# Kernel optimization log

Measured on AMD Instinct MI355X. Metric: run time of the kernel, lower is better.

Reference implementation:

```python
import jax, jax.numpy as jnp
import numpy as np

S = 64.0
M = 0.5
EPS = 1e-07
NORM_EPS = 1e-12  # matches torch F.normalize default eps
B, D, C = 512, 512, 64000


def _l2_normalize(a, axis=-1):
    n = jnp.sqrt(jnp.sum(a * a, axis=axis, keepdims=True))
    return a / jnp.maximum(n, NORM_EPS)


def setup_inputs() -> dict:
    key = jax.random.key(0)
    kx, ky, kw = jax.random.split(key, 3)
    x = jax.random.normal(kx, (B, D), dtype=jnp.float32)
    y = jax.random.randint(ky, (B,), 0, C, dtype=jnp.int64)
    # kaiming_uniform-ish init: bound = sqrt(6 / fan_in)
    bound = np.sqrt(6.0 / D).astype(np.float32)
    W = jax.random.uniform(kw, (C, D), dtype=jnp.float32, minval=-bound, maxval=bound)
    return {"x": x, "y": y, "W": W}


def reference(x, y, W):
    # cosine similarities: [B, C]
    theta = _l2_normalize(x) @ _l2_normalize(W).T
    # target logit per row
    tgt = jnp.take_along_axis(theta, y[:, None], axis=1)[:, 0]  # [B]
    numerator = S * jnp.cos(jnp.arccos(jnp.clip(tgt, -1.0 + EPS, 1.0 - EPS)) + M)
    # sum of exp(s*theta) over non-target classes (mask out target column)
    is_tgt = jnp.arange(C, dtype=y.dtype)[None, :] == y[:, None]  # [B, C]
    excl_sum = jnp.sum(jnp.where(is_tgt, 0.0, jnp.exp(S * theta)), axis=1)  # [B]
    denominator = jnp.exp(numerator) + excl_sum
    return -jnp.mean(numerator - jnp.log(denominator))
```

## Files before the change

### kernel.cpp

```cpp
#include <hip/hip_runtime.h>


#define B_N 512
#define D_N 512
#define C_N 64000
#define S_SCALE 64.0f
#define MARGIN 0.5f
#define EPS_C 1e-7f

typedef unsigned short ushort_t;
typedef __attribute__((ext_vector_type(8))) short short8;
typedef __attribute__((ext_vector_type(4))) float floatx4;

__device__ __forceinline__ ushort_t f2bf(float f) {
    unsigned int u = __float_as_uint(f);
    u += 0x7fffu + ((u >> 16) & 1u);
    return (ushort_t)(u >> 16);
}

__global__ void xprep_kernel(const float* __restrict__ x,
                             ushort_t* __restrict__ xn,
                             float* __restrict__ rowsum) {
    int b = blockIdx.x;
    int t = threadIdx.x;
    if (b == 128) {
        rowsum[t] = 0.0f;
        rowsum[t + 256] = 0.0f;
        return;
    }
    int row  = b * 4 + (t >> 6);
    int lane = t & 63;
    const float4* p = (const float4*)(x + (size_t)row * D_N);
    float4 v0 = p[lane];
    float4 v1 = p[lane + 64];
    float ss = v0.x*v0.x + v0.y*v0.y + v0.z*v0.z + v0.w*v0.w
             + v1.x*v1.x + v1.y*v1.y + v1.z*v1.z + v1.w*v1.w;
#pragma unroll
    for (int off = 32; off > 0; off >>= 1) ss += __shfl_xor(ss, off);
    float sc = 1.0f / fmaxf(sqrtf(ss), 1e-12f);
    ushort_t* dst = xn + (size_t)row * D_N;
    uint2 o0, o1;
    o0.x = (unsigned)f2bf(v0.x*sc) | ((unsigned)f2bf(v0.y*sc) << 16);
    o0.y = (unsigned)f2bf(v0.z*sc) | ((unsigned)f2bf(v0.w*sc) << 16);
    o1.x = (unsigned)f2bf(v1.x*sc) | ((unsigned)f2bf(v1.y*sc) << 16);
    o1.y = (unsigned)f2bf(v1.z*sc) | ((unsigned)f2bf(v1.w*sc) << 16);
    *(uint2*)(dst + lane * 4)       = o0;
    *(uint2*)(dst + 256 + lane * 4) = o1;
}

__device__ __forceinline__ void g2lds16(const ushort_t* g, ushort_t* l) {
    __builtin_amdgcn_global_load_lds(
        (const __attribute__((address_space(1))) void*)g,
        (__attribute__((address_space(3))) void*)l, 16, 0, 0);
}

__global__ __launch_bounds__(512, 2)
void gemm_fused_kernel(const float* __restrict__ W,
                       const ushort_t* __restrict__ xn,
                       const int* __restrict__ y,
                       float* __restrict__ rowsum,
                       float* __restrict__ tgt) {
    __shared__ ushort_t sW[64 * 512];
    __shared__ ushort_t sA[2 * 512 * 32];

    int t    = threadIdx.x;
    int lane = t & 63;
    int w    = t >> 6;
    int lq   = lane >> 4;
    int lc   = lane & 15;
    int cn0  = blockIdx.x * 64;

#pragma unroll
    for (int rr = 0; rr < 8; ++rr) {
        int row = w * 8 + rr;
        const float4* p = (const float4*)(W + (size_t)(cn0 + row) * D_N);
        float4 a = p[lane * 2];
        float4 b = p[lane * 2 + 1];
        float ss = a.x*a.x + a.y*a.y + a.z*a.z + a.w*a.w
                 + b.x*b.x + b.y*b.y + b.z*b.z + b.w*b.w;
#pragma unroll
        for (int off = 32; off > 0; off >>= 1) ss += __shfl_xor(ss, off);
        float sc = 1.0f / fmaxf(sqrtf(ss), 1e-12f);
        uint4 o;
        o.x = (unsigned)f2bf(a.x*sc) | ((unsigned)f2bf(a.y*sc) << 16);
        o.y = (unsigned)f2bf(a.z*sc) | ((unsigned)f2bf(a.w*sc) << 16);
        o.z = (unsigned)f2bf(b.x*sc) | ((unsigned)f2bf(b.y*sc) << 16);
        o.w = (unsigned)f2bf(b.z*sc) | ((unsigned)f2bf(b.w*sc) << 16);
        int kc = lane;
        int rs = row ^ (kc & 7);
        *((uint4*)(sW + kc * 512 + rs * 8)) = o;
    }

    const ushort_t* gA = xn + (size_t)(t >> 2) * D_N + (t & 3) * 8;
#pragma unroll
    for (int c = 0; c < 4; ++c)
        g2lds16(gA + (size_t)c * 128 * D_N, sA + (t + c * 512) * 8);
    __syncthreads();

    floatx4 acc[4][4];
#pragma unroll
    for (int i = 0; i < 4; i++)
#pragma unroll
        for (int j = 0; j < 4; j++) acc[i][j] = (floatx4){0.f, 0.f, 0.f, 0.f};

    int fragA_base = (w * 64 + lc) * 32 + lq * 8;

    for (int k = 0; k < 16; ++k) {
        int cur = (k & 1) * 16384;
        if (k < 15) {
            int nxt = ((k + 1) & 1) * 16384;
            int kk  = (k + 1) * 32;
#pragma unroll
            for (int c = 0; c < 4; ++c)
                g2lds16(gA + (size_t)c * 128 * D_N + kk,
                        sA + nxt + (t + c * 512) * 8);
        }
        short8 af[4], bfr[4];
#pragma unroll
        for (int tm = 0; tm < 4; tm++)
            af[tm] = *(const short8*)(sA + cur + fragA_base + tm * 512);
#pragma unroll
        for (int tn = 0; tn < 4; tn++) {
            int kc = k * 4 + lq;
            int rs = (tn * 16 + lc) ^ (kc & 7);
            bfr[tn] = *(const short8*)(sW + kc * 512 + rs * 8);
        }
#pragma unroll
        for (int tm = 0; tm < 4; tm++)
#pragma unroll
            for (int tn = 0; tn < 4; tn++)
                acc[tm][tn] = __builtin_amdgcn_mfma_f32_16x16x32_bf16(
                    af[tm], bfr[tn], acc[tm][tn], 0, 0, 0);
        __syncthreads();
    }

    float* rowacc = (float*)sA;
#pragma unroll
    for (int tm = 0; tm < 4; tm++) {
#pragma unroll
        for (int r = 0; r < 4; r++) {
            int lrow = w * 64 + tm * 16 + lq * 4 + r;
            int yv   = y[lrow];
            float esum = 0.0f;
#pragma unroll
            for (int tn = 0; tn < 4; tn++) {
                int gcol = cn0 + tn * 16 + lc;
                float theta = acc[tm][tn][r];
                if (gcol == yv) {
                    tgt[lrow] = theta;
                } else {
                    esum += __expf(S_SCALE * theta);
                }
            }
#pragma unroll
            for (int off = 1; off < 16; off <<= 1) esum += __shfl_xor(esum, off);
            if (lc == 0) rowacc[lrow] = esum;
        }
    }
    __syncthreads();
    atomicAdd(&rowsum[t], rowacc[t]);
}

__global__ void finalize_kernel(const float* __restrict__ rowsum,
                                const float* __restrict__ tgt,
                                float* __restrict__ out) {
    __shared__ float red[256];
    int t = threadIdx.x;
    float s = 0.0f;
    for (int r = t; r < B_N; r += 256) {
        float tv = tgt[r];
        tv = fminf(fmaxf(tv, -1.0f + EPS_C), 1.0f - EPS_C);
        float num = S_SCALE * cosf(acosf(tv) + MARGIN);
        float den = expf(num) + rowsum[r];
        s += num - logf(den);
    }
    red[t] = s;
    __syncthreads();
    for (int o = 128; o > 0; o >>= 1) {
        if (t < o) red[t] += red[t + o];
        __syncthreads();
    }
    if (t == 0) out[0] = -red[0] / (float)B_N;
}

extern "C" void kernel_launch(void* const* d_in, const int* in_sizes, int n_in,
                              void* d_out, int out_size, void* d_ws, size_t ws_size,
                              hipStream_t stream) {
    const float* x = (const float*)d_in[0];
    const int*   y = (const int*)d_in[1];
    const float* W = (const float*)d_in[2];
    float* out = (float*)d_out;

    char* ws = (char*)d_ws;
    ushort_t* xn = (ushort_t*)ws;
    float* rowsum = (float*)(ws + 524288);
    float* tgt    = rowsum + B_N;

    xprep_kernel<<<129, 256, 0, stream>>>(x, xn, rowsum);
    gemm_fused_kernel<<<C_N / 64, 512, 0, stream>>>(W, xn, y, rowsum, tgt);
    finalize_kernel<<<1, 256, 0, stream>>>(rowsum, tgt, out);
}
```

Measured before the change: 269.4 us.

## Read x fragments directly from global, drop A LDS staging, replicate rowsum atomics

The GEMM kernel no longer stages the normalized x tile through double-buffered LDS. Each wave reads its A fragments straight from global memory (L2-resident), which removes the per-k-step barriers and halves LDS use, and the launch bound is raised to 4 blocks per CU. The per-row atomic accumulation is spread across 16 replicated rowsum buffers keyed by block index to cut atomic contention, and the finalize kernel sums the replicas. The trade-off is more global/L2 traffic and latency on the A loads, with no prefetch to hide it.

```diff
diff --git a/kernel.cpp b/kernel.cpp
--- a/kernel.cpp
+++ b/kernel.cpp
@@ -7,6 +7,7 @@
 #define S_SCALE 64.0f
 #define MARGIN 0.5f
 #define EPS_C 1e-7f
+#define NREP 16
 
 typedef unsigned short ushort_t;
 typedef __attribute__((ext_vector_type(8))) short short8;
@@ -20,12 +21,13 @@
 
 __global__ void xprep_kernel(const float* __restrict__ x,
                              ushort_t* __restrict__ xn,
-                             float* __restrict__ rowsum) {
+                             float* __restrict__ rowsumR) {
     int b = blockIdx.x;
     int t = threadIdx.x;
     if (b == 128) {
-        rowsum[t] = 0.0f;
-        rowsum[t + 256] = 0.0f;
+#pragma unroll
+        for (int i = 0; i < NREP * B_N / 256; ++i)
+            rowsumR[i * 256 + t] = 0.0f;
         return;
     }
     int row  = b * 4 + (t >> 6);
@@ -48,20 +50,13 @@
     *(uint2*)(dst + 256 + lane * 4) = o1;
 }
 
-__device__ __forceinline__ void g2lds16(const ushort_t* g, ushort_t* l) {
-    __builtin_amdgcn_global_load_lds(
-        (const __attribute__((address_space(1))) void*)g,
-        (__attribute__((address_space(3))) void*)l, 16, 0, 0);
-}
-
-__global__ __launch_bounds__(512, 2)
+__global__ __launch_bounds__(512, 4)
 void gemm_fused_kernel(const float* __restrict__ W,
                        const ushort_t* __restrict__ xn,
                        const int* __restrict__ y,
-                       float* __restrict__ rowsum,
+                       float* __restrict__ rowsumR,
                        float* __restrict__ tgt) {
     __shared__ ushort_t sW[64 * 512];
-    __shared__ ushort_t sA[2 * 512 * 32];
 
     int t    = threadIdx.x;
     int lane = t & 63;
@@ -90,11 +85,6 @@
         int rs = row ^ (kc & 7);
         *((uint4*)(sW + kc * 512 + rs * 8)) = o;
     }
-
-    const ushort_t* gA = xn + (size_t)(t >> 2) * D_N + (t & 3) * 8;
-#pragma unroll
-    for (int c = 0; c < 4; ++c)
-        g2lds16(gA + (size_t)c * 128 * D_N, sA + (t + c * 512) * 8);
     __syncthreads();
 
     floatx4 acc[4][4];
@@ -103,25 +93,19 @@
 #pragma unroll
         for (int j = 0; j < 4; j++) acc[i][j] = (floatx4){0.f, 0.f, 0.f, 0.f};
 
-    int fragA_base = (w * 64 + lc) * 32 + lq * 8;
+    const ushort_t* rowp[4];
+#pragma unroll
+    for (int tm = 0; tm < 4; tm++)
+        rowp[tm] = xn + (size_t)(w * 64 + tm * 16 + lc) * D_N + lq * 8;
 
     for (int k = 0; k < 16; ++k) {
-        int cur = (k & 1) * 16384;
-        if (k < 15) {
-            int nxt = ((k + 1) & 1) * 16384;
-            int kk  = (k + 1) * 32;
-#pragma unroll
-            for (int c = 0; c < 4; ++c)
-                g2lds16(gA + (size_t)c * 128 * D_N + kk,
-                        sA + nxt + (t + c * 512) * 8);
-        }
         short8 af[4], bfr[4];
 #pragma unroll
         for (int tm = 0; tm < 4; tm++)
-            af[tm] = *(const short8*)(sA + cur + fragA_base + tm * 512);
+            af[tm] = *(const short8*)(rowp[tm] + k * 32);
+        int kc = k * 4 + lq;
 #pragma unroll
         for (int tn = 0; tn < 4; tn++) {
-            int kc = k * 4 + lq;
             int rs = (tn * 16 + lc) ^ (kc & 7);
             bfr[tn] = *(const short8*)(sW + kc * 512 + rs * 8);
         }
@@ -131,10 +115,10 @@
             for (int tn = 0; tn < 4; tn++)
                 acc[tm][tn] = __builtin_amdgcn_mfma_f32_16x16x32_bf16(
                     af[tm], bfr[tn], acc[tm][tn], 0, 0, 0);
-        __syncthreads();
     }
 
-    float* rowacc = (float*)sA;
+    __syncthreads();
+    float* rowacc = (float*)sW;
 #pragma unroll
     for (int tm = 0; tm < 4; tm++) {
 #pragma unroll
@@ -158,20 +142,23 @@
         }
     }
     __syncthreads();
-    atomicAdd(&rowsum[t], rowacc[t]);
+    atomicAdd(&rowsumR[(blockIdx.x & (NREP - 1)) * B_N + t], rowacc[t]);
 }
 
-__global__ void finalize_kernel(const float* __restrict__ rowsum,
+__global__ void finalize_kernel(const float* __restrict__ rowsumR,
                                 const float* __restrict__ tgt,
                                 float* __restrict__ out) {
     __shared__ float red[256];
     int t = threadIdx.x;
     float s = 0.0f;
     for (int r = t; r < B_N; r += 256) {
+        float rs = 0.0f;
+#pragma unroll
+        for (int i = 0; i < NREP; ++i) rs += rowsumR[i * B_N + r];
         float tv = tgt[r];
         tv = fminf(fmaxf(tv, -1.0f + EPS_C), 1.0f - EPS_C);
         float num = S_SCALE * cosf(acosf(tv) + MARGIN);
-        float den = expf(num) + rowsum[r];
+        float den = expf(num) + rs;
         s += num - logf(den);
     }
     red[t] = s;
@@ -192,11 +179,11 @@
     float* out = (float*)d_out;
 
     char* ws = (char*)d_ws;
-    ushort_t* xn = (ushort_t*)ws;
-    float* rowsum = (float*)(ws + 524288);
-    float* tgt    = rowsum + B_N;
+    ushort_t* xn    = (ushort_t*)ws;
+    float* rowsumR  = (float*)(ws + 524288);
+    float* tgt      = rowsumR + NREP * B_N;
 
-    xprep_kernel<<<129, 256, 0, stream>>>(x, xn, rowsum);
-    gemm_fused_kernel<<<C_N / 64, 512, 0, stream>>>(W, xn, y, rowsum, tgt);
-    finalize_kernel<<<1, 256, 0, stream>>>(rowsum, tgt, out);
+    xprep_kernel<<<129, 256, 0, stream>>>(x, xn, rowsumR);
+    gemm_fused_kernel<<<C_N / 64, 512, 0, stream>>>(W, xn, y, rowsumR, tgt);
+    finalize_kernel<<<1, 256, 0, stream>>>(rowsumR, tgt, out);
 }
```

After: 261.7 us. 2.9% less time.
